# Kernel tuning notes

Measured on AMD Instinct MI355X. Metric: run time of the kernel, lower is better.

Reference implementation:

```python
import jax, jax.numpy as jnp
import numpy as np

T = 1.0  # temperature from __init__


def setup_inputs() -> dict:
    key = jax.random.key(0)
    k1, k2, k3, k4, k5 = jax.random.split(key, 5)
    N, C, NC = 128, 2048, 50000
    Kp, Kn = 4, 508
    inputs = jax.random.normal(k1, (N, C), dtype=jnp.float32)
    positive_index = jax.random.randint(k2, (N, Kp), 0, NC, dtype=jnp.int64)
    negative_index = jax.random.randint(k3, (N, Kn), 0, NC, dtype=jnp.int64)
    cof = jax.random.uniform(k4, (Kp,), dtype=jnp.float32)
    # memory bank buffer (registered buffer M); L2-normalized rows like after updates
    M = jax.random.normal(k5, (NC, C), dtype=jnp.float32)
    M = M / jnp.linalg.norm(M, axis=1, keepdims=True)
    return {"inputs": inputs, "positive_index": positive_index,
            "negative_index": negative_index, "cof": cof, "M": M}


def reference(inputs, positive_index, negative_index, cof, M):
    # index_list: [N, K] with K = Kp + Kn
    index_list = jnp.concatenate([positive_index, negative_index], axis=1)
    # fused gather + batched matmul: logits[n, k] = inputs[n] . M[index_list[n, k]]
    Mg = M[index_list]                                   # [N, K, C] gather
    logits = jnp.einsum('nc,nkc->nk', inputs, Mg) * T    # [N, K]
    # the Python loop over j reuses identical logits; only the CE target column varies
    logp = jax.nn.log_softmax(logits, axis=1)            # [N, K]
    Kp = positive_index.shape[1]
    # loss = sum_j cof[j] * cross_entropy(logits, target=j) = -sum_j cof[j]*mean_n logp[n, j]
    loss = -jnp.sum(cof * jnp.mean(logp[:, :Kp], axis=0))
    return loss, logits
```

## Files before the change

kernel.cpp:

```cpp
#include <hip/hip_runtime.h>

constexpr int N    = 128;
constexpr int C    = 2048;
constexpr int KP   = 4;
constexpr int KN   = 508;
constexpr int K    = 512;
constexpr int NK   = N * K;
constexpr int NC   = 50000;
constexpr int MAXD = 16;
constexpr int OCAP = 512;


__device__ __forceinline__ int gather_idx(const int* pos_idx, const int* neg_idx, int n, int k) {
    return (k < KP) ? pos_idx[n * KP + k] : neg_idx[n * KN + (k - KP)];
}

__global__ __launch_bounds__(256) void zero_kernel(int* __restrict__ count, int* __restrict__ ocount) {
    const int t = blockIdx.x * 256 + threadIdx.x;
    if (t < NC) count[t] = 0;
    if (t == 0) *ocount = 0;
}

__global__ __launch_bounds__(256) void build_kernel(
    const int* __restrict__ pos_idx, const int* __restrict__ neg_idx,
    int* __restrict__ count, int* __restrict__ pairs,
    int* __restrict__ ocount, int* __restrict__ overflow)
{
    const int t = blockIdx.x * 256 + threadIdx.x;
    const int n = t >> 9, k = t & (K - 1);
    const int idx = gather_idx(pos_idx, neg_idx, n, k);
    const int packed = (n << 9) | k;
    const int p = atomicAdd(&count[idx], 1);
    if (p < MAXD) {
        pairs[idx * MAXD + p] = packed;
    } else {
        const int o = atomicAdd(ocount, 1);
        if (o < OCAP) overflow[o] = (idx << 16) | packed;
    }
}

__global__ __launch_bounds__(256) void gemv_dedup_kernel(
    const float* __restrict__ inputs,
    const float* __restrict__ M,
    const int*   __restrict__ count,
    const int*   __restrict__ pairs,
    const int*   __restrict__ ocount,
    const int*   __restrict__ overflow,
    float*       __restrict__ logits)
{
    const int wave = threadIdx.x >> 6;
    const int lane = threadIdx.x & 63;
    const int idx  = blockIdx.x * 4 + wave;
    if (idx >= NC) return;

    const int cnt = count[idx];
    if (cnt == 0) return;

    const float4* __restrict__ b = reinterpret_cast<const float4*>(M + (size_t)idx * C);
    float4 mrow[8];
    #pragma unroll
    for (int i = 0; i < 8; ++i) mrow[i] = b[i * 64 + lane];

    const float4* __restrict__ A = reinterpret_cast<const float4*>(inputs);

    auto dot_and_store = [&](int packed) {
        const int n = packed >> 9, k = packed & (K - 1);
        const float4* __restrict__ a = A + (size_t)n * (C / 4);
        float acc = 0.f;
        #pragma unroll
        for (int i = 0; i < 8; ++i) {
            float4 av = a[i * 64 + lane];
            float4 bv = mrow[i];
            acc = fmaf(av.x, bv.x, acc);
            acc = fmaf(av.y, bv.y, acc);
            acc = fmaf(av.z, bv.z, acc);
            acc = fmaf(av.w, bv.w, acc);
        }
        #pragma unroll
        for (int off = 32; off > 0; off >>= 1)
            acc += __shfl_down(acc, off, 64);
        if (lane == 0) logits[n * K + k] = acc;
    };

    const int lim = cnt < MAXD ? cnt : MAXD;
    for (int j = 0; j < lim; ++j)
        dot_and_store(pairs[idx * MAXD + j]);

    if (cnt > MAXD) {
        const int oc = min(*ocount, OCAP);
        for (int i = 0; i < oc; ++i) {
            const int e = overflow[i];
            if ((e >> 16) == idx) dot_and_store(e & 0xFFFF);
        }
    }
}

__global__ __launch_bounds__(256) void logits_kernel(
    const float* __restrict__ inputs,
    const int*   __restrict__ pos_idx,
    const int*   __restrict__ neg_idx,
    const float* __restrict__ M,
    float*       __restrict__ logits)
{
    const int wave = threadIdx.x >> 6;
    const int lane = threadIdx.x & 63;
    const int n    = blockIdx.y;
    const int k    = (blockIdx.x << 2) + wave;

    const int idx = (k < KP) ? pos_idx[n * KP + k]
                             : neg_idx[n * KN + (k - KP)];

    const float4* __restrict__ a = reinterpret_cast<const float4*>(inputs + (size_t)n * C);
    const float4* __restrict__ b = reinterpret_cast<const float4*>(M + (size_t)idx * C);

    float acc = 0.f;
    #pragma unroll
    for (int i = 0; i < C / (4 * 64); ++i) {
        float4 av = a[i * 64 + lane];
        float4 bv = b[i * 64 + lane];
        acc = fmaf(av.x, bv.x, acc);
        acc = fmaf(av.y, bv.y, acc);
        acc = fmaf(av.z, bv.z, acc);
        acc = fmaf(av.w, bv.w, acc);
    }
    #pragma unroll
    for (int off = 32; off > 0; off >>= 1)
        acc += __shfl_down(acc, off, 64);
    if (lane == 0) logits[n * K + k] = acc;
}

__global__ __launch_bounds__(512) void softmax_loss_kernel(
    const float* __restrict__ logits,
    const float* __restrict__ cof,
    float*       __restrict__ row_loss)
{
    __shared__ float red[8];
    __shared__ float xs[KP];
    const int n    = blockIdx.x;
    const int t    = threadIdx.x;
    const int wid  = t >> 6;
    const int lane = t & 63;

    float x = logits[n * K + t];

    float m = x;
    #pragma unroll
    for (int off = 1; off < 64; off <<= 1)
        m = fmaxf(m, __shfl_xor(m, off, 64));
    if (lane == 0) red[wid] = m;
    __syncthreads();
    float bm = red[0];
    #pragma unroll
    for (int i = 1; i < 8; ++i) bm = fmaxf(bm, red[i]);

    float s = expf(x - bm);
    #pragma unroll
    for (int off = 1; off < 64; off <<= 1)
        s += __shfl_xor(s, off, 64);
    __syncthreads();
    if (lane == 0) red[wid] = s;
    if (t < KP) xs[t] = x;
    __syncthreads();

    if (t == 0) {
        float bs = 0.f;
        #pragma unroll
        for (int i = 0; i < 8; ++i) bs += red[i];
        const float logZ = bm + logf(bs);
        float acc = 0.f;
        #pragma unroll
        for (int j = 0; j < KP; ++j)
            acc += cof[j] * (xs[j] - logZ);
        row_loss[n] = acc;
    }
}

__global__ __launch_bounds__(128) void loss_reduce_kernel(
    const float* __restrict__ row_loss,
    float*       __restrict__ out)
{
    const int t = threadIdx.x;
    float v = row_loss[t];
    #pragma unroll
    for (int off = 1; off < 64; off <<= 1)
        v += __shfl_xor(v, off, 64);
    __shared__ float red[2];
    if ((t & 63) == 0) red[t >> 6] = v;
    __syncthreads();
    if (t == 0) out[0] = -(red[0] + red[1]) / (float)N;
}

extern "C" void kernel_launch(void* const* d_in, const int* in_sizes, int n_in,
                              void* d_out, int out_size, void* d_ws, size_t ws_size,
                              hipStream_t stream) {
    const float* inputs  = (const float*)d_in[0];
    const int*   pos_idx = (const int*)d_in[1];
    const int*   neg_idx = (const int*)d_in[2];
    const float* cof     = (const float*)d_in[3];
    const float* M       = (const float*)d_in[4];

    float* out    = (float*)d_out;
    float* logits = out + 1;

    const size_t need = (size_t)(NC + NC * MAXD + 1 + OCAP + N) * 4;
    if (ws_size >= need) {
        int*   count    = (int*)d_ws;
        int*   pairs    = count + NC;
        int*   ocount   = pairs + (size_t)NC * MAXD;
        int*   overflow = ocount + 1;
        float* row_loss = (float*)(overflow + OCAP);

        zero_kernel<<<(NC + 255) / 256, 256, 0, stream>>>(count, ocount);
        build_kernel<<<NK / 256, 256, 0, stream>>>(pos_idx, neg_idx, count, pairs, ocount, overflow);
        gemv_dedup_kernel<<<(NC + 3) / 4, 256, 0, stream>>>(inputs, M, count, pairs, ocount, overflow, logits);
        softmax_loss_kernel<<<N, K, 0, stream>>>(logits, cof, row_loss);
        loss_reduce_kernel<<<1, N, 0, stream>>>(row_loss, out);
    } else {
        float* row_loss = (float*)d_ws;
        logits_kernel<<<dim3(K / 4, N), 256, 0, stream>>>(inputs, pos_idx, neg_idx, M, logits);
        softmax_loss_kernel<<<N, K, 0, stream>>>(logits, cof, row_loss);
        loss_reduce_kernel<<<1, N, 0, stream>>>(row_loss, out);
    }
}
```

Baseline: 83.98 us.

## Compact unique bank rows into a worklist and memset counters instead of zero kernel

The build kernel now appends each first-seen bank row index to a compact worklist. The GEMV kernel then assigns waves to worklist entries instead of scanning all 50000 rows, most of which are unused. The zero kernel is replaced by a hipMemsetAsync over the count and header region. The pair list is preloaded as an int4, and the dot product uses two accumulators. The worklist is filled in atomic order, which scatters M row accesses and adds one more atomic per unique row; grid size stays at NC/4, so many blocks still exit early.

```diff
diff --git a/kernel.cpp b/kernel.cpp
--- a/kernel.cpp
+++ b/kernel.cpp
@@ -10,21 +10,16 @@
 constexpr int MAXD = 16;
 constexpr int OCAP = 512;
 
+constexpr int HDR_INTS = NC + 2;
 
 __device__ __forceinline__ int gather_idx(const int* pos_idx, const int* neg_idx, int n, int k) {
     return (k < KP) ? pos_idx[n * KP + k] : neg_idx[n * KN + (k - KP)];
 }
 
-__global__ __launch_bounds__(256) void zero_kernel(int* __restrict__ count, int* __restrict__ ocount) {
-    const int t = blockIdx.x * 256 + threadIdx.x;
-    if (t < NC) count[t] = 0;
-    if (t == 0) *ocount = 0;
-}
-
 __global__ __launch_bounds__(256) void build_kernel(
     const int* __restrict__ pos_idx, const int* __restrict__ neg_idx,
-    int* __restrict__ count, int* __restrict__ pairs,
-    int* __restrict__ ocount, int* __restrict__ overflow)
+    int* __restrict__ count, int* __restrict__ ocount, int* __restrict__ wcount,
+    int* __restrict__ pairs, int* __restrict__ work, int* __restrict__ overflow)
 {
     const int t = blockIdx.x * 256 + threadIdx.x;
     const int n = t >> 9, k = t & (K - 1);
@@ -37,6 +32,10 @@
         const int o = atomicAdd(ocount, 1);
         if (o < OCAP) overflow[o] = (idx << 16) | packed;
     }
+    if (p == 0) {
+        const int w = atomicAdd(wcount, 1);
+        work[w] = idx;
+    }
 }
 
 __global__ __launch_bounds__(256) void gemv_dedup_kernel(
@@ -44,38 +43,46 @@
     const float* __restrict__ M,
     const int*   __restrict__ count,
     const int*   __restrict__ pairs,
+    const int*   __restrict__ work,
+    const int*   __restrict__ wcount,
     const int*   __restrict__ ocount,
     const int*   __restrict__ overflow,
     float*       __restrict__ logits)
 {
     const int wave = threadIdx.x >> 6;
     const int lane = threadIdx.x & 63;
-    const int idx  = blockIdx.x * 4 + wave;
-    if (idx >= NC) return;
-
-    const int cnt = count[idx];
-    if (cnt == 0) return;
+    const int g    = blockIdx.x * 4 + wave;
+    if (g >= *wcount) return;
+
+    const int idx = work[g];
 
     const float4* __restrict__ b = reinterpret_cast<const float4*>(M + (size_t)idx * C);
     float4 mrow[8];
     #pragma unroll
     for (int i = 0; i < 8; ++i) mrow[i] = b[i * 64 + lane];
+
+    const int4* __restrict__ pl = reinterpret_cast<const int4*>(&pairs[idx * MAXD]);
+    int4 p0 = pl[0];
+    const int cnt = count[idx];
 
     const float4* __restrict__ A = reinterpret_cast<const float4*>(inputs);
 
     auto dot_and_store = [&](int packed) {
         const int n = packed >> 9, k = packed & (K - 1);
         const float4* __restrict__ a = A + (size_t)n * (C / 4);
-        float acc = 0.f;
-        #pragma unroll
-        for (int i = 0; i < 8; ++i) {
-            float4 av = a[i * 64 + lane];
-            float4 bv = mrow[i];
-            acc = fmaf(av.x, bv.x, acc);
-            acc = fmaf(av.y, bv.y, acc);
-            acc = fmaf(av.z, bv.z, acc);
-            acc = fmaf(av.w, bv.w, acc);
+        float acc0 = 0.f, acc1 = 0.f;
+        #pragma unroll
+        for (int i = 0; i < 8; i += 2) {
+            float4 av0 = a[i * 64 + lane];
+            float4 av1 = a[(i + 1) * 64 + lane];
+            float4 bv0 = mrow[i];
+            float4 bv1 = mrow[i + 1];
+            acc0 = fmaf(av0.x, bv0.x, acc0); acc1 = fmaf(av1.x, bv1.x, acc1);
+            acc0 = fmaf(av0.y, bv0.y, acc0); acc1 = fmaf(av1.y, bv1.y, acc1);
+            acc0 = fmaf(av0.z, bv0.z, acc0); acc1 = fmaf(av1.z, bv1.z, acc1);
+            acc0 = fmaf(av0.w, bv0.w, acc0); acc1 = fmaf(av1.w, bv1.w, acc1);
         }
+        float acc = acc0 + acc1;
         #pragma unroll
         for (int off = 32; off > 0; off >>= 1)
             acc += __shfl_down(acc, off, 64);
@@ -83,7 +90,11 @@
     };
 
     const int lim = cnt < MAXD ? cnt : MAXD;
-    for (int j = 0; j < lim; ++j)
+    if (lim > 0) dot_and_store(p0.x);
+    if (lim > 1) dot_and_store(p0.y);
+    if (lim > 2) dot_and_store(p0.z);
+    if (lim > 3) dot_and_store(p0.w);
+    for (int j = 4; j < lim; ++j)
         dot_and_store(pairs[idx * MAXD + j]);
 
     if (cnt > MAXD) {
@@ -93,6 +104,67 @@
             if ((e >> 16) == idx) dot_and_store(e & 0xFFFF);
         }
     }
+}
+
+__global__ __launch_bounds__(512) void softmax_loss_kernel(
+    const float* __restrict__ logits,
+    const float* __restrict__ cof,
+    float*       __restrict__ row_loss)
+{
+    __shared__ float red[8];
+    __shared__ float xs[KP];
+    const int n    = blockIdx.x;
+    const int t    = threadIdx.x;
+    const int wid  = t >> 6;
+    const int lane = t & 63;
+
+    float x = logits[n * K + t];
+
+    float m = x;
+    #pragma unroll
+    for (int off = 1; off < 64; off <<= 1)
+        m = fmaxf(m, __shfl_xor(m, off, 64));
+    if (lane == 0) red[wid] = m;
+    __syncthreads();
+    float bm = red[0];
+    #pragma unroll
+    for (int i = 1; i < 8; ++i) bm = fmaxf(bm, red[i]);
+
+    float s = expf(x - bm);
+    #pragma unroll
+    for (int off = 1; off < 64; off <<= 1)
+        s += __shfl_xor(s, off, 64);
+    __syncthreads();
+    if (lane == 0) red[wid] = s;
+    if (t < KP) xs[t] = x;
+    __syncthreads();
+
+    if (t == 0) {
+        float bs = 0.f;
+        #pragma unroll
+        for (int i = 0; i < 8; ++i) bs += red[i];
+        const float logZ = bm + logf(bs);
+        float acc = 0.f;
+        #pragma unroll
+        for (int j = 0; j < KP; ++j)
+            acc += cof[j] * (xs[j] - logZ);
+        row_loss[n] = acc;
+    }
+}
+
+__global__ __launch_bounds__(128) void loss_reduce_kernel(
+    const float* __restrict__ row_loss,
+    float*       __restrict__ out)
+{
+    const int t = threadIdx.x;
+    float v = row_loss[t];
+    #pragma unroll
+    for (int off = 1; off < 64; off <<= 1)
+        v += __shfl_xor(v, off, 64);
+    __shared__ float red[2];
+    if ((t & 63) == 0) red[t >> 6] = v;
+    __syncthreads();
+    if (t == 0) out[0] = -(red[0] + red[1]) / (float)N;
 }
 
 __global__ __launch_bounds__(256) void logits_kernel(
@@ -127,67 +199,6 @@
     for (int off = 32; off > 0; off >>= 1)
         acc += __shfl_down(acc, off, 64);
     if (lane == 0) logits[n * K + k] = acc;
-}
-
-__global__ __launch_bounds__(512) void softmax_loss_kernel(
-    const float* __restrict__ logits,
-    const float* __restrict__ cof,
-    float*       __restrict__ row_loss)
-{
-    __shared__ float red[8];
-    __shared__ float xs[KP];
-    const int n    = blockIdx.x;
-    const int t    = threadIdx.x;
-    const int wid  = t >> 6;
-    const int lane = t & 63;
-
-    float x = logits[n * K + t];
-
-    float m = x;
-    #pragma unroll
-    for (int off = 1; off < 64; off <<= 1)
-        m = fmaxf(m, __shfl_xor(m, off, 64));
-    if (lane == 0) red[wid] = m;
-    __syncthreads();
-    float bm = red[0];
-    #pragma unroll
-    for (int i = 1; i < 8; ++i) bm = fmaxf(bm, red[i]);
-
-    float s = expf(x - bm);
-    #pragma unroll
-    for (int off = 1; off < 64; off <<= 1)
-        s += __shfl_xor(s, off, 64);
-    __syncthreads();
-    if (lane == 0) red[wid] = s;
-    if (t < KP) xs[t] = x;
-    __syncthreads();
-
-    if (t == 0) {
-        float bs = 0.f;
-        #pragma unroll
-        for (int i = 0; i < 8; ++i) bs += red[i];
-        const float logZ = bm + logf(bs);
-        float acc = 0.f;
-        #pragma unroll
-        for (int j = 0; j < KP; ++j)
-            acc += cof[j] * (xs[j] - logZ);
-        row_loss[n] = acc;
-    }
-}
-
-__global__ __launch_bounds__(128) void loss_reduce_kernel(
-    const float* __restrict__ row_loss,
-    float*       __restrict__ out)
-{
-    const int t = threadIdx.x;
-    float v = row_loss[t];
-    #pragma unroll
-    for (int off = 1; off < 64; off <<= 1)
-        v += __shfl_xor(v, off, 64);
-    __shared__ float red[2];
-    if ((t & 63) == 0) red[t >> 6] = v;
-    __syncthreads();
-    if (t == 0) out[0] = -(red[0] + red[1]) / (float)N;
 }
 
 extern "C" void kernel_launch(void* const* d_in, const int* in_sizes, int n_in,
@@ -202,17 +213,21 @@
     float* out    = (float*)d_out;
     float* logits = out + 1;
 
-    const size_t need = (size_t)(NC + NC * MAXD + 1 + OCAP + N) * 4;
+    const size_t need = (size_t)(HDR_INTS + (size_t)NC * MAXD + NC + OCAP + N) * 4;
     if (ws_size >= need) {
         int*   count    = (int*)d_ws;
-        int*   pairs    = count + NC;
-        int*   ocount   = pairs + (size_t)NC * MAXD;
-        int*   overflow = ocount + 1;
+        int*   ocount   = count + NC;
+        int*   wcount   = ocount + 1;
+        int*   pairs    = count + HDR_INTS;
+        int*   work     = pairs + (size_t)NC * MAXD;
+        int*   overflow = work + NC;
         float* row_loss = (float*)(overflow + OCAP);
 
-        zero_kernel<<<(NC + 255) / 256, 256, 0, stream>>>(count, ocount);
-        build_kernel<<<NK / 256, 256, 0, stream>>>(pos_idx, neg_idx, count, pairs, ocount, overflow);
-        gemv_dedup_kernel<<<(NC + 3) / 4, 256, 0, stream>>>(inputs, M, count, pairs, ocount, overflow, logits);
+        hipMemsetAsync(count, 0, (size_t)HDR_INTS * 4, stream);
+        build_kernel<<<NK / 256, 256, 0, stream>>>(pos_idx, neg_idx, count, ocount, wcount,
+                                                   pairs, work, overflow);
+        gemv_dedup_kernel<<<(NC + 3) / 4, 256, 0, stream>>>(inputs, M, count, pairs, work,
+                                                            wcount, ocount, overflow, logits);
         softmax_loss_kernel<<<N, K, 0, stream>>>(logits, cof, row_loss);
         loss_reduce_kernel<<<1, N, 0, stream>>>(row_loss, out);
     } else {
```

Result: slower. 88.25 us (+5.1%).

## Build compacted work list of index groups for dedup gather-GEMV

Applied to the files above, without the earlier changes.

The build step now appends a work item for every group of up to four (n,k) pairs that share a memory-bank row. The GEMV kernel then launches one wave per work item instead of one per bank row, so empty rows no longer occupy waves. Each wave streams the M row once and computes up to four dot products with templated accumulators. The zero kernel is replaced by hipMemsetAsync, and the overflow path is dropped in favour of MAXD=32. The risk is that rows referenced more than 32 times silently lose logits, and the grid is sized NK/4+16 with most waves exiting early.

```diff
diff --git a/kernel.cpp b/kernel.cpp
--- a/kernel.cpp
+++ b/kernel.cpp
@@ -7,92 +7,165 @@
 constexpr int K    = 512;
 constexpr int NK   = N * K;
 constexpr int NC   = 50000;
-constexpr int MAXD = 16;
-constexpr int OCAP = 512;
-
+constexpr int MAXD = 32;
+constexpr int GRP  = 4;
+
+constexpr int HDR_INTS = NC + 1;
 
 __device__ __forceinline__ int gather_idx(const int* pos_idx, const int* neg_idx, int n, int k) {
     return (k < KP) ? pos_idx[n * KP + k] : neg_idx[n * KN + (k - KP)];
 }
 
-__global__ __launch_bounds__(256) void zero_kernel(int* __restrict__ count, int* __restrict__ ocount) {
-    const int t = blockIdx.x * 256 + threadIdx.x;
-    if (t < NC) count[t] = 0;
-    if (t == 0) *ocount = 0;
-}
-
 __global__ __launch_bounds__(256) void build_kernel(
     const int* __restrict__ pos_idx, const int* __restrict__ neg_idx,
-    int* __restrict__ count, int* __restrict__ pairs,
-    int* __restrict__ ocount, int* __restrict__ overflow)
+    int* __restrict__ count, int* __restrict__ wcount,
+    int* __restrict__ pairs, int* __restrict__ work)
 {
     const int t = blockIdx.x * 256 + threadIdx.x;
     const int n = t >> 9, k = t & (K - 1);
     const int idx = gather_idx(pos_idx, neg_idx, n, k);
-    const int packed = (n << 9) | k;
     const int p = atomicAdd(&count[idx], 1);
     if (p < MAXD) {
-        pairs[idx * MAXD + p] = packed;
-    } else {
-        const int o = atomicAdd(ocount, 1);
-        if (o < OCAP) overflow[o] = (idx << 16) | packed;
-    }
-}
-
-__global__ __launch_bounds__(256) void gemv_dedup_kernel(
+        pairs[idx * MAXD + p] = (n << 9) | k;
+        if ((p & (GRP - 1)) == 0) {
+            const int w = atomicAdd(wcount, 1);
+            work[w] = (idx << 3) | (p >> 2);
+        }
+    }
+}
+
+template<int MM>
+__device__ __forceinline__ void serve_group(
+    const float4* __restrict__ b,
+    const float4* __restrict__ A,
+    const int*    pk,
+    float*        __restrict__ logits,
+    int lane)
+{
+    const float4* a[MM];
+    float acc[MM];
+    #pragma unroll
+    for (int j = 0; j < MM; ++j) {
+        a[j]   = A + (size_t)(pk[j] >> 9) * (C / 4);
+        acc[j] = 0.f;
+    }
+    #pragma unroll 4
+    for (int i = 0; i < 8; ++i) {
+        const float4 mv = b[i * 64];
+        #pragma unroll
+        for (int j = 0; j < MM; ++j) {
+            const float4 av = a[j][i * 64];
+            acc[j] = fmaf(mv.x, av.x, acc[j]);
+            acc[j] = fmaf(mv.y, av.y, acc[j]);
+            acc[j] = fmaf(mv.z, av.z, acc[j]);
+            acc[j] = fmaf(mv.w, av.w, acc[j]);
+        }
+    }
+    #pragma unroll
+    for (int j = 0; j < MM; ++j) {
+        float v = acc[j];
+        #pragma unroll
+        for (int off = 32; off > 0; off >>= 1)
+            v += __shfl_down(v, off, 64);
+        if (lane == 0)
+            logits[(pk[j] >> 9) * K + (pk[j] & (K - 1))] = v;
+    }
+}
+
+__global__ __launch_bounds__(256, 8) void gemv_dedup_kernel(
     const float* __restrict__ inputs,
     const float* __restrict__ M,
     const int*   __restrict__ count,
     const int*   __restrict__ pairs,
-    const int*   __restrict__ ocount,
-    const int*   __restrict__ overflow,
+    const int*   __restrict__ work,
+    const int*   __restrict__ wcount,
     float*       __restrict__ logits)
 {
     const int wave = threadIdx.x >> 6;
     const int lane = threadIdx.x & 63;
-    const int idx  = blockIdx.x * 4 + wave;
-    if (idx >= NC) return;
-
-    const int cnt = count[idx];
-    if (cnt == 0) return;
-
-    const float4* __restrict__ b = reinterpret_cast<const float4*>(M + (size_t)idx * C);
-    float4 mrow[8];
-    #pragma unroll
-    for (int i = 0; i < 8; ++i) mrow[i] = b[i * 64 + lane];
-
-    const float4* __restrict__ A = reinterpret_cast<const float4*>(inputs);
-
-    auto dot_and_store = [&](int packed) {
-        const int n = packed >> 9, k = packed & (K - 1);
-        const float4* __restrict__ a = A + (size_t)n * (C / 4);
+    const int g    = blockIdx.x * 4 + wave;
+    if (g >= *wcount) return;
+
+    const int item = work[g];
+    const int idx  = item >> 3;
+    const int grp  = item & 7;
+    const int cnt  = count[idx];
+    int m = cnt - (grp << 2);
+    m = m > GRP ? GRP : m;
+
+    const int4 pp = *reinterpret_cast<const int4*>(&pairs[idx * MAXD + (grp << 2)]);
+    const int  pk[4] = {pp.x, pp.y, pp.z, pp.w};
+
+    const float4* b = reinterpret_cast<const float4*>(M + (size_t)idx * C) + lane;
+    const float4* A = reinterpret_cast<const float4*>(inputs) + lane;
+
+    switch (m) {
+        case 1: serve_group<1>(b, A, pk, logits, lane); break;
+        case 2: serve_group<2>(b, A, pk, logits, lane); break;
+        case 3: serve_group<3>(b, A, pk, logits, lane); break;
+        default: serve_group<4>(b, A, pk, logits, lane); break;
+    }
+}
+
+__global__ __launch_bounds__(512) void softmax_loss_kernel(
+    const float* __restrict__ logits,
+    const float* __restrict__ cof,
+    float*       __restrict__ row_loss)
+{
+    __shared__ float red[8];
+    __shared__ float xs[KP];
+    const int n    = blockIdx.x;
+    const int t    = threadIdx.x;
+    const int wid  = t >> 6;
+    const int lane = t & 63;
+
+    float x = logits[n * K + t];
+
+    float m = x;
+    #pragma unroll
+    for (int off = 1; off < 64; off <<= 1)
+        m = fmaxf(m, __shfl_xor(m, off, 64));
+    if (lane == 0) red[wid] = m;
+    __syncthreads();
+    float bm = red[0];
+    #pragma unroll
+    for (int i = 1; i < 8; ++i) bm = fmaxf(bm, red[i]);
+
+    float s = expf(x - bm);
+    #pragma unroll
+    for (int off = 1; off < 64; off <<= 1)
+        s += __shfl_xor(s, off, 64);
+    __syncthreads();
+    if (lane == 0) red[wid] = s;
+    if (t < KP) xs[t] = x;
+    __syncthreads();
+
+    if (t == 0) {
+        float bs = 0.f;
+        #pragma unroll
+        for (int i = 0; i < 8; ++i) bs += red[i];
+        const float logZ = bm + logf(bs);
         float acc = 0.f;
         #pragma unroll
-        for (int i = 0; i < 8; ++i) {
-            float4 av = a[i * 64 + lane];
-            float4 bv = mrow[i];
-            acc = fmaf(av.x, bv.x, acc);
-            acc = fmaf(av.y, bv.y, acc);
-            acc = fmaf(av.z, bv.z, acc);
-            acc = fmaf(av.w, bv.w, acc);
-        }
-        #pragma unroll
-        for (int off = 32; off > 0; off >>= 1)
-            acc += __shfl_down(acc, off, 64);
-        if (lane == 0) logits[n * K + k] = acc;
-    };
-
-    const int lim = cnt < MAXD ? cnt : MAXD;
-    for (int j = 0; j < lim; ++j)
-        dot_and_store(pairs[idx * MAXD + j]);
-
-    if (cnt > MAXD) {
-        const int oc = min(*ocount, OCAP);
-        for (int i = 0; i < oc; ++i) {
-            const int e = overflow[i];
-            if ((e >> 16) == idx) dot_and_store(e & 0xFFFF);
-        }
-    }
+        for (int j = 0; j < KP; ++j)
+            acc += cof[j] * (xs[j] - logZ);
+        row_loss[n] = acc;
+    }
+}
+
+__global__ __launch_bounds__(128) void loss_reduce_kernel(
+    const float* __restrict__ row_loss,
+    float*       __restrict__ out)
+{
+    const int t = threadIdx.x;
+    float v = row_loss[t];
+    #pragma unroll
+    for (int off = 1; off < 64; off <<= 1)
+        v += __shfl_xor(v, off, 64);
+    __shared__ float red[2];
+    if ((t & 63) == 0) red[t >> 6] = v;
+    __syncthreads();
+    if (t == 0) out[0] = -(red[0] + red[1]) / (float)N;
 }
 
 __global__ __launch_bounds__(256) void logits_kernel(
@@ -127,67 +200,6 @@
     for (int off = 32; off > 0; off >>= 1)
         acc += __shfl_down(acc, off, 64);
     if (lane == 0) logits[n * K + k] = acc;
-}
-
-__global__ __launch_bounds__(512) void softmax_loss_kernel(
-    const float* __restrict__ logits,
-    const float* __restrict__ cof,
-    float*       __restrict__ row_loss)
-{
-    __shared__ float red[8];
-    __shared__ float xs[KP];
-    const int n    = blockIdx.x;
-    const int t    = threadIdx.x;
-    const int wid  = t >> 6;
-    const int lane = t & 63;
-
-    float x = logits[n * K + t];
-
-    float m = x;
-    #pragma unroll
-    for (int off = 1; off < 64; off <<= 1)
-        m = fmaxf(m, __shfl_xor(m, off, 64));
-    if (lane == 0) red[wid] = m;
-    __syncthreads();
-    float bm = red[0];
-    #pragma unroll
-    for (int i = 1; i < 8; ++i) bm = fmaxf(bm, red[i]);
-
-    float s = expf(x - bm);
-    #pragma unroll
-    for (int off = 1; off < 64; off <<= 1)
-        s += __shfl_xor(s, off, 64);
-    __syncthreads();
-    if (lane == 0) red[wid] = s;
-    if (t < KP) xs[t] = x;
-    __syncthreads();
-
-    if (t == 0) {
-        float bs = 0.f;
-        #pragma unroll
-        for (int i = 0; i < 8; ++i) bs += red[i];
-        const float logZ = bm + logf(bs);
-        float acc = 0.f;
-        #pragma unroll
-        for (int j = 0; j < KP; ++j)
-            acc += cof[j] * (xs[j] - logZ);
-        row_loss[n] = acc;
-    }
-}
-
-__global__ __launch_bounds__(128) void loss_reduce_kernel(
-    const float* __restrict__ row_loss,
-    float*       __restrict__ out)
-{
-    const int t = threadIdx.x;
-    float v = row_loss[t];
-    #pragma unroll
-    for (int off = 1; off < 64; off <<= 1)
-        v += __shfl_xor(v, off, 64);
-    __shared__ float red[2];
-    if ((t & 63) == 0) red[t >> 6] = v;
-    __syncthreads();
-    if (t == 0) out[0] = -(red[0] + red[1]) / (float)N;
 }
 
 extern "C" void kernel_launch(void* const* d_in, const int* in_sizes, int n_in,
@@ -202,17 +214,17 @@
     float* out    = (float*)d_out;
     float* logits = out + 1;
 
-    const size_t need = (size_t)(NC + NC * MAXD + 1 + OCAP + N) * 4;
+    const size_t need = (size_t)(HDR_INTS + (size_t)NC * MAXD + (NK + 64) + N) * 4;
     if (ws_size >= need) {
         int*   count    = (int*)d_ws;
-        int*   pairs    = count + NC;
-        int*   ocount   = pairs + (size_t)NC * MAXD;
-        int*   overflow = ocount + 1;
-        float* row_loss = (float*)(overflow + OCAP);
-
-        zero_kernel<<<(NC + 255) / 256, 256, 0, stream>>>(count, ocount);
-        build_kernel<<<NK / 256, 256, 0, stream>>>(pos_idx, neg_idx, count, pairs, ocount, overflow);
-        gemv_dedup_kernel<<<(NC + 3) / 4, 256, 0, stream>>>(inputs, M, count, pairs, ocount, overflow, logits);
+        int*   wcount   = count + NC;
+        int*   pairs    = count + HDR_INTS;
+        int*   work     = pairs + (size_t)NC * MAXD;
+        float* row_loss = (float*)(work + NK + 64);
+
+        hipMemsetAsync(count, 0, (size_t)HDR_INTS * 4, stream);
+        build_kernel<<<NK / 256, 256, 0, stream>>>(pos_idx, neg_idx, count, wcount, pairs, work);
+        gemv_dedup_kernel<<<NK / 4 + 16, 256, 0, stream>>>(inputs, M, count, pairs, work, wcount, logits);
         softmax_loss_kernel<<<N, K, 0, stream>>>(logits, cof, row_loss);
         loss_reduce_kernel<<<1, N, 0, stream>>>(row_loss, out);
     } else {
```

After: 93.59 us. +11.4%, slower.

## Compact work list and inline slots for dedup GEMV with persistent grid

Applied to the files above, without the earlier changes.

The build step now appends each distinct memory-bank row to a compact work list and stores up to three (n,k) pairs inline next to the count in a 16-byte slot, with a separate overflow array and a global spill list. The GEMV becomes a grid-stride persistent kernel over the work list with 1024 blocks, so it no longer launches a wave per bank row (12500 blocks) only for most to exit early. The zeroing kernel is replaced by hipMemsetAsync over the slot array and counters. This adds atomic contention on the work counter and a larger memset in exchange for fewer idle waves and fewer scattered pair loads.

```diff
diff --git a/kernel.cpp b/kernel.cpp
--- a/kernel.cpp
+++ b/kernel.cpp
@@ -7,126 +7,104 @@
 constexpr int K    = 512;
 constexpr int NK   = N * K;
 constexpr int NC   = 50000;
-constexpr int MAXD = 16;
-constexpr int OCAP = 512;
-
+constexpr int NINL = 3;
+constexpr int NOVF = 13;
+constexpr int MAXD = NINL + NOVF;
+constexpr int SCAP = 2048;
+
+constexpr size_t MEMSET_INTS = (size_t)NC * 4 + 2;
 
 __device__ __forceinline__ int gather_idx(const int* pos_idx, const int* neg_idx, int n, int k) {
     return (k < KP) ? pos_idx[n * KP + k] : neg_idx[n * KN + (k - KP)];
 }
 
-__global__ __launch_bounds__(256) void zero_kernel(int* __restrict__ count, int* __restrict__ ocount) {
-    const int t = blockIdx.x * 256 + threadIdx.x;
-    if (t < NC) count[t] = 0;
-    if (t == 0) *ocount = 0;
-}
-
 __global__ __launch_bounds__(256) void build_kernel(
     const int* __restrict__ pos_idx, const int* __restrict__ neg_idx,
-    int* __restrict__ count, int* __restrict__ pairs,
-    int* __restrict__ ocount, int* __restrict__ overflow)
+    int* __restrict__ slot, int* __restrict__ wcount, int* __restrict__ scount,
+    int* __restrict__ ovf, int* __restrict__ work, int* __restrict__ spill)
 {
     const int t = blockIdx.x * 256 + threadIdx.x;
     const int n = t >> 9, k = t & (K - 1);
     const int idx = gather_idx(pos_idx, neg_idx, n, k);
     const int packed = (n << 9) | k;
-    const int p = atomicAdd(&count[idx], 1);
-    if (p < MAXD) {
-        pairs[idx * MAXD + p] = packed;
+    const int p = atomicAdd(&slot[idx * 4], 1);
+    if (p == 0) {
+        work[atomicAdd(wcount, 1)] = idx;
+    }
+    if (p < NINL) {
+        slot[idx * 4 + 1 + p] = packed;
+    } else if (p < MAXD) {
+        ovf[idx * NOVF + (p - NINL)] = packed;
     } else {
-        const int o = atomicAdd(ocount, 1);
-        if (o < OCAP) overflow[o] = (idx << 16) | packed;
+        const int s = atomicAdd(scount, 1);
+        if (s < SCAP) spill[s] = (idx << 16) | packed;
     }
 }
 
 __global__ __launch_bounds__(256) void gemv_dedup_kernel(
     const float* __restrict__ inputs,
     const float* __restrict__ M,
-    const int*   __restrict__ count,
-    const int*   __restrict__ pairs,
-    const int*   __restrict__ ocount,
-    const int*   __restrict__ overflow,
+    const int*   __restrict__ slot,
+    const int*   __restrict__ ovf,
+    const int*   __restrict__ work,
+    const int*   __restrict__ wcount,
+    const int*   __restrict__ scount,
+    const int*   __restrict__ spill,
     float*       __restrict__ logits)
 {
-    const int wave = threadIdx.x >> 6;
     const int lane = threadIdx.x & 63;
-    const int idx  = blockIdx.x * 4 + wave;
-    if (idx >= NC) return;
-
-    const int cnt = count[idx];
-    if (cnt == 0) return;
-
-    const float4* __restrict__ b = reinterpret_cast<const float4*>(M + (size_t)idx * C);
-    float4 mrow[8];
-    #pragma unroll
-    for (int i = 0; i < 8; ++i) mrow[i] = b[i * 64 + lane];
+    const int wid  = (blockIdx.x * 256 + threadIdx.x) >> 6;
+    const int nw   = gridDim.x * 4;
+    const int W    = *wcount;
 
     const float4* __restrict__ A = reinterpret_cast<const float4*>(inputs);
 
-    auto dot_and_store = [&](int packed) {
-        const int n = packed >> 9, k = packed & (K - 1);
-        const float4* __restrict__ a = A + (size_t)n * (C / 4);
-        float acc = 0.f;
+    int next_idx = (wid < W) ? work[wid] : 0;
+
+    for (int g = wid; g < W; g += nw) {
+        const int idx = next_idx;
+        if (g + nw < W) next_idx = work[g + nw];
+
+        const int4 s = *reinterpret_cast<const int4*>(&slot[idx * 4]);
+        const int cnt = s.x;
+
+        const float4* __restrict__ b = reinterpret_cast<const float4*>(M + (size_t)idx * C);
+        float4 mrow[8];
         #pragma unroll
-        for (int i = 0; i < 8; ++i) {
-            float4 av = a[i * 64 + lane];
-            float4 bv = mrow[i];
-            acc = fmaf(av.x, bv.x, acc);
-            acc = fmaf(av.y, bv.y, acc);
-            acc = fmaf(av.z, bv.z, acc);
-            acc = fmaf(av.w, bv.w, acc);
+        for (int i = 0; i < 8; ++i) mrow[i] = b[i * 64 + lane];
+
+        auto serve = [&](int packed) {
+            const float4* __restrict__ a = A + (size_t)(packed >> 9) * (C / 4);
+            float acc = 0.f;
+            #pragma unroll
+            for (int i = 0; i < 8; ++i) {
+                const float4 av = a[i * 64 + lane];
+                acc = fmaf(mrow[i].x, av.x, acc);
+                acc = fmaf(mrow[i].y, av.y, acc);
+                acc = fmaf(mrow[i].z, av.z, acc);
+                acc = fmaf(mrow[i].w, av.w, acc);
+            }
+            #pragma unroll
+            for (int off = 32; off > 0; off >>= 1)
+                acc += __shfl_down(acc, off, 64);
+            if (lane == 0)
+                logits[(packed >> 9) * K + (packed & (K - 1))] = acc;
+        };
+
+        serve(s.y);
+        if (cnt > 1) serve(s.z);
+        if (cnt > 2) serve(s.w);
+        const int lim = cnt < MAXD ? cnt : MAXD;
+        for (int j = NINL; j < lim; ++j)
+            serve(ovf[idx * NOVF + (j - NINL)]);
+        if (cnt > MAXD) {
+            const int sc = min(*scount, SCAP);
+            for (int i = 0; i < sc; ++i) {
+                const int e = spill[i];
+                if ((e >> 16) == idx) serve(e & 0xFFFF);
+            }
         }
-        #pragma unroll
-        for (int off = 32; off > 0; off >>= 1)
-            acc += __shfl_down(acc, off, 64);
-        if (lane == 0) logits[n * K + k] = acc;
-    };
-
-    const int lim = cnt < MAXD ? cnt : MAXD;
-    for (int j = 0; j < lim; ++j)
-        dot_and_store(pairs[idx * MAXD + j]);
-
-    if (cnt > MAXD) {
-        const int oc = min(*ocount, OCAP);
-        for (int i = 0; i < oc; ++i) {
-            const int e = overflow[i];
-            if ((e >> 16) == idx) dot_and_store(e & 0xFFFF);
-        }
-    }
-}
-
-__global__ __launch_bounds__(256) void logits_kernel(
-    const float* __restrict__ inputs,
-    const int*   __restrict__ pos_idx,
-    const int*   __restrict__ neg_idx,
-    const float* __restrict__ M,
-    float*       __restrict__ logits)
-{
-    const int wave = threadIdx.x >> 6;
-    const int lane = threadIdx.x & 63;
-    const int n    = blockIdx.y;
-    const int k    = (blockIdx.x << 2) + wave;
-
-    const int idx = (k < KP) ? pos_idx[n * KP + k]
-                             : neg_idx[n * KN + (k - KP)];
-
-    const float4* __restrict__ a = reinterpret_cast<const float4*>(inputs + (size_t)n * C);
-    const float4* __restrict__ b = reinterpret_cast<const float4*>(M + (size_t)idx * C);
-
-    float acc = 0.f;
-    #pragma unroll
-    for (int i = 0; i < C / (4 * 64); ++i) {
-        float4 av = a[i * 64 + lane];
-        float4 bv = b[i * 64 + lane];
-        acc = fmaf(av.x, bv.x, acc);
-        acc = fmaf(av.y, bv.y, acc);
-        acc = fmaf(av.z, bv.z, acc);
-        acc = fmaf(av.w, bv.w, acc);
-    }
-    #pragma unroll
-    for (int off = 32; off > 0; off >>= 1)
-        acc += __shfl_down(acc, off, 64);
-    if (lane == 0) logits[n * K + k] = acc;
+    }
 }
 
 __global__ __launch_bounds__(512) void softmax_loss_kernel(
@@ -190,6 +168,40 @@
     if (t == 0) out[0] = -(red[0] + red[1]) / (float)N;
 }
 
+__global__ __launch_bounds__(256) void logits_kernel(
+    const float* __restrict__ inputs,
+    const int*   __restrict__ pos_idx,
+    const int*   __restrict__ neg_idx,
+    const float* __restrict__ M,
+    float*       __restrict__ logits)
+{
+    const int wave = threadIdx.x >> 6;
+    const int lane = threadIdx.x & 63;
+    const int n    = blockIdx.y;
+    const int k    = (blockIdx.x << 2) + wave;
+
+    const int idx = (k < KP) ? pos_idx[n * KP + k]
+                             : neg_idx[n * KN + (k - KP)];
+
+    const float4* __restrict__ a = reinterpret_cast<const float4*>(inputs + (size_t)n * C);
+    const float4* __restrict__ b = reinterpret_cast<const float4*>(M + (size_t)idx * C);
+
+    float acc = 0.f;
+    #pragma unroll
+    for (int i = 0; i < C / (4 * 64); ++i) {
+        float4 av = a[i * 64 + lane];
+        float4 bv = b[i * 64 + lane];
+        acc = fmaf(av.x, bv.x, acc);
+        acc = fmaf(av.y, bv.y, acc);
+        acc = fmaf(av.z, bv.z, acc);
+        acc = fmaf(av.w, bv.w, acc);
+    }
+    #pragma unroll
+    for (int off = 32; off > 0; off >>= 1)
+        acc += __shfl_down(acc, off, 64);
+    if (lane == 0) logits[n * K + k] = acc;
+}
+
 extern "C" void kernel_launch(void* const* d_in, const int* in_sizes, int n_in,
                               void* d_out, int out_size, void* d_ws, size_t ws_size,
                               hipStream_t stream) {
@@ -202,17 +214,21 @@
     float* out    = (float*)d_out;
     float* logits = out + 1;
 
-    const size_t need = (size_t)(NC + NC * MAXD + 1 + OCAP + N) * 4;
+    const size_t need = (MEMSET_INTS + (size_t)NC * NOVF + NC + SCAP + N) * 4;
     if (ws_size >= need) {
-        int*   count    = (int*)d_ws;
-        int*   pairs    = count + NC;
-        int*   ocount   = pairs + (size_t)NC * MAXD;
-        int*   overflow = ocount + 1;
-        float* row_loss = (float*)(overflow + OCAP);
-
-        zero_kernel<<<(NC + 255) / 256, 256, 0, stream>>>(count, ocount);
-        build_kernel<<<NK / 256, 256, 0, stream>>>(pos_idx, neg_idx, count, pairs, ocount, overflow);
-        gemv_dedup_kernel<<<(NC + 3) / 4, 256, 0, stream>>>(inputs, M, count, pairs, ocount, overflow, logits);
+        int*   slot     = (int*)d_ws;
+        int*   wcount   = slot + (size_t)NC * 4;
+        int*   scount   = wcount + 1;
+        int*   ovf      = scount + 1;
+        int*   work     = ovf + (size_t)NC * NOVF;
+        int*   spill    = work + NC;
+        float* row_loss = (float*)(spill + SCAP);
+
+        hipMemsetAsync(slot, 0, MEMSET_INTS * 4, stream);
+        build_kernel<<<NK / 256, 256, 0, stream>>>(pos_idx, neg_idx, slot, wcount, scount,
+                                                   ovf, work, spill);
+        gemv_dedup_kernel<<<1024, 256, 0, stream>>>(inputs, M, slot, ovf, work,
+                                                    wcount, scount, spill, logits);
         softmax_loss_kernel<<<N, K, 0, stream>>>(logits, cof, row_loss);
         loss_reduce_kernel<<<1, N, 0, stream>>>(row_loss, out);
     } else {
```

Measured after the change: 105.3 us. 1.25x slower.
